# Kernel tuning notes

Measured on AMD Instinct MI355X. Metric: run time of the kernel, lower is better.

The kernel has to match this reference:

```python
import jax, jax.numpy as jnp
import numpy as np

B, X, Y, Z, C = 1, 16, 16, 16, 768
NUM_HEADS = 12


def setup_inputs() -> dict:
    key = jax.random.key(0)
    k0, k1, k2 = jax.random.split(key, 3)
    x = jax.random.normal(k0, (B, X, Y, Z, C), dtype=jnp.float32)
    # Linear weights stored as [in, out] (torch stores [out, in]; math is x @ W_in_out + b)
    w_qkv = jax.random.normal(k1, (C, 3 * C), dtype=jnp.float32) * 0.02
    b_qkv = jnp.zeros((3 * C,), dtype=jnp.float32)
    w_proj = jax.random.normal(k2, (C, C), dtype=jnp.float32) * 0.02
    b_proj = jnp.zeros((C,), dtype=jnp.float32)
    return {"x": x, "w_qkv": w_qkv, "b_qkv": b_qkv, "w_proj": w_proj, "b_proj": b_proj}


def reference(x, w_qkv, b_qkv, w_proj, b_proj):
    b, xx, yy, zz, c = x.shape
    h = NUM_HEADS
    hd = c // h
    scale = hd ** (-0.5)
    n = xx * yy * zz  # flatten 3D grid into tokens

    qkv = x.reshape(b, n, c) @ w_qkv + b_qkv          # [B, N, 3C]
    qkv = qkv.reshape(b, n, 3, h, hd).transpose(2, 0, 3, 1, 4)  # [3, B, H, N, hd]
    q, k, v = qkv[0], qkv[1], qkv[2]

    attn = jnp.einsum('bhnd,bhmd->bhnm', q * scale, k)  # [B, H, N, N]
    attn = jax.nn.softmax(attn, axis=-1)
    out = jnp.einsum('bhnm,bhmd->bhnd', attn, v)        # [B, H, N, hd]
    out = out.transpose(0, 2, 1, 3).reshape(b, n, c)
    out = out @ w_proj + b_proj
    return out.reshape(b, xx, yy, zz, c)
```

## Files before the change

### kernel.cpp

```cpp
#include <hip/hip_runtime.h>
#include <cstddef>

#define N_TOK 4096
#define C_DIM 768
#define H_NUM 12
#define C3    2304

typedef unsigned short u16;
using short8  = __attribute__((ext_vector_type(8))) short;
using floatx4 = __attribute__((ext_vector_type(4))) float;
using u16x4   = __attribute__((ext_vector_type(4))) u16;
using uint2v  = __attribute__((ext_vector_type(2))) unsigned;

#define K2SCALE 0.18033688011112043f

__device__ __forceinline__ u16 f2bf(float f) {
  union { float f; unsigned u; } v; v.f = f;
  unsigned r = v.u + 0x7FFFu + ((v.u >> 16) & 1u);
  return (u16)(r >> 16);
}

__device__ __forceinline__ unsigned permpack(float a, float b) {
  union { float f; unsigned u; } x, y; x.f = a; y.f = b;
  return __builtin_amdgcn_perm(y.u, x.u, 0x07060302u);
}

__device__ __forceinline__ float aexp2(float x) {
  float r;
  asm("v_exp_f32 %0, %1" : "=v"(r) : "v"(x));
  return r;
}

__device__ __forceinline__ float arcp(float x) {
  float r;
  asm("v_rcp_f32 %0, %1" : "=v"(r) : "v"(x));
  return r;
}

__device__ __forceinline__ void gload_lds16(const void* g, void* l) {
  __builtin_amdgcn_global_load_lds(
      (const __attribute__((address_space(1))) unsigned int*)g,
      (__attribute__((address_space(3))) unsigned int*)l, 16, 0, 0);
}

__global__ void k_pre(const float* __restrict__ x, u16* __restrict__ xb,
                      const float* __restrict__ wq, u16* __restrict__ wqT,
                      const float* __restrict__ wp, u16* __restrict__ wpT) {
  __shared__ float tile[32][33];
  const int b = blockIdx.x;
  if (b < 3072) {
    int i = b * 256 + threadIdx.x;
    float4 f = ((const float4*)x)[i];
    u16x4 o;
    o[0] = f2bf(f.x); o[1] = f2bf(f.y); o[2] = f2bf(f.z); o[3] = f2bf(f.w);
    ((u16x4*)xb)[i] = o;
    return;
  }
  const float* in; u16* out; int Cc, bx, by;
  if (b < 4800) { int t = b - 3072; in = wq; out = wqT; Cc = 2304; bx = t % 72; by = t / 72; }
  else          { int t = b - 4800; in = wp; out = wpT; Cc = 768;  bx = t % 24; by = t / 24; }
  const int R = 768;
  const int tx = threadIdx.x & 31;
  const int ty = threadIdx.x >> 5;
  const int c0 = bx * 32, r0 = by * 32;
#pragma unroll
  for (int i = 0; i < 32; i += 8)
    tile[ty + i][tx] = in[(size_t)(r0 + ty + i) * Cc + c0 + tx];
  __syncthreads();
#pragma unroll
  for (int i = 0; i < 32; i += 8)
    out[(size_t)(c0 + ty + i) * R + r0 + tx] = f2bf(tile[tx][ty + i]);
}

template <int MODE>
__global__ __launch_bounds__(256)
void k_gemm_bt(const u16* __restrict__ A, const u16* __restrict__ B,
               const float* __restrict__ bias, void* __restrict__ outp,
               u16* __restrict__ vT, int K) {
  __shared__ u16 As[128 * 32];
  __shared__ u16 Bs[128 * 32];
  const int tid  = threadIdx.x;
  const int wave = tid >> 6, lane = tid & 63, quad = lane >> 4, l16 = lane & 15;
  const int wrow = wave >> 1, wcol = wave & 1;
  const int bm = blockIdx.y, bn = blockIdx.x;
  const int r3 = l16 & 3;

  floatx4 acc[4][4];
#pragma unroll
  for (int i = 0; i < 4; ++i)
#pragma unroll
    for (int j = 0; j < 4; ++j)
#pragma unroll
      for (int r = 0; r < 4; ++r) acc[i][j][r] = 0.f;

  const int ar = tid >> 2;
  const int ac = ((tid & 3) ^ (ar & 3)) * 8;
  const u16* gA = A + (size_t)(bm * 128 + ar) * K + ac;
  const u16* gB = B + (size_t)(bn * 128 + ar) * K + ac;
  u16* lA = &As[0] + tid * 8;
  u16* lB = &Bs[0] + tid * 8;

  for (int k0 = 0; k0 < K; k0 += 32) {
    gload_lds16(gA + k0,                  lA);
    gload_lds16(gA + k0 + (size_t)64 * K, lA + 2048);
    gload_lds16(gB + k0,                  lB);
    gload_lds16(gB + k0 + (size_t)64 * K, lB + 2048);
    __syncthreads();
    short8 af[4], bf[4];
#pragma unroll
    for (int t = 0; t < 4; ++t) {
      af[t] = *(const short8*)&As[(wrow * 64 + t * 16 + l16) * 32 + ((quad ^ r3) * 8)];
      bf[t] = *(const short8*)&Bs[(wcol * 64 + t * 16 + l16) * 32 + ((quad ^ r3) * 8)];
    }
#pragma unroll
    for (int tm = 0; tm < 4; ++tm)
#pragma unroll
      for (int tn = 0; tn < 4; ++tn)
        acc[tm][tn] = __builtin_amdgcn_mfma_f32_16x16x32_bf16(af[tm], bf[tn], acc[tm][tn], 0, 0, 0);
    __syncthreads();
  }

  if (MODE == 0) {
    u16* qkv = (u16*)outp;
    const float qs = (bn < 6) ? K2SCALE : 1.0f;
#pragma unroll
    for (int tn = 0; tn < 4; ++tn) {
      const int col = bn * 128 + wcol * 64 + tn * 16 + l16;
      const float bc = bias[col];
      if (col < 1536) {
#pragma unroll
        for (int tm = 0; tm < 4; ++tm) {
          const int rowb = bm * 128 + wrow * 64 + tm * 16 + quad * 4;
#pragma unroll
          for (int r = 0; r < 4; ++r)
            qkv[(size_t)(rowb + r) * C3 + col] = f2bf((acc[tm][tn][r] + bc) * qs);
        }
      } else {
        const int hd_ = col - 1536;
#pragma unroll
        for (int tm = 0; tm < 4; ++tm) {
          const int rowb = bm * 128 + wrow * 64 + tm * 16 + quad * 4;
          u16x4 pk;
#pragma unroll
          for (int r = 0; r < 4; ++r) pk[r] = f2bf(acc[tm][tn][r] + bc);
          *(u16x4*)&vT[(size_t)hd_ * N_TOK + rowb] = pk;
        }
      }
    }
  } else {
    float* out = (float*)outp;
#pragma unroll
    for (int tn = 0; tn < 4; ++tn) {
      const int col = bn * 128 + wcol * 64 + tn * 16 + l16;
      const float bc = bias[col];
#pragma unroll
      for (int tm = 0; tm < 4; ++tm) {
        const int rowb = bm * 128 + wrow * 64 + tm * 16 + quad * 4;
#pragma unroll
        for (int r = 0; r < 4; ++r)
          out[(size_t)(rowb + r) * C_DIM + col] = acc[tm][tn][r] + bc;
      }
    }
  }
}

__global__ __launch_bounds__(256)
void k_flash(const u16* __restrict__ qkv, const u16* __restrict__ vT,
             float* __restrict__ Opart, float* __restrict__ lpart) {
  __shared__ u16 Ks[2][64 * 64];
  __shared__ u16 Vs[2][64 * 64];
  __shared__ u16 Ps[4][32 * 64];
  const int tid  = threadIdx.x;
  const int wave = tid >> 6, lane = tid & 63, quad = lane >> 4, l16 = lane & 15;
  const int qt = blockIdx.x, h = blockIdx.y, split = blockIdx.z;
  const int lr = tid >> 3;
  const int lc = ((tid & 7) ^ (lr & 7)) * 8;
  const int r7 = l16 & 7;
  const int kb = split * 2048;

  short8 bq[2][2];
#pragma unroll
  for (int qs = 0; qs < 2; ++qs)
#pragma unroll
    for (int ks = 0; ks < 2; ++ks)
      bq[qs][ks] = *(const short8*)&qkv[(size_t)(qt * 128 + wave * 32 + qs * 16 + l16) * C3
                                        + h * 64 + ks * 32 + quad * 8];

  const u16* gk = qkv + (size_t)lr * C3 + C_DIM + h * 64 + lc;
  const u16* gv = vT + (size_t)(h * 64 + lr) * N_TOK + lc;

  auto stage = [&](int b, int m0) {
#pragma unroll
    for (int p = 0; p < 2; ++p) {
      gload_lds16(gk + (size_t)(m0 + p * 32) * C3,    &Ks[b][p * 2048 + tid * 8]);
      gload_lds16(gv + (size_t)(p * 32) * N_TOK + m0, &Vs[b][p * 2048 + tid * 8]);
    }
  };

  floatx4 o0[4], o1[4], l0, l1, zv;
#pragma unroll
  for (int r = 0; r < 4; ++r) { zv[r] = 0.f; l0[r] = 0.f; l1[r] = 0.f; }
#pragma unroll
  for (int d = 0; d < 4; ++d)
#pragma unroll
    for (int r = 0; r < 4; ++r) { o0[d][r] = 0.f; o1[d][r] = 0.f; }

  short8 ones;
#pragma unroll
  for (int i = 0; i < 8; ++i) ones[i] = (short)0x3F80;

  u16* psw = &Ps[wave][0];

  auto compute = [&](int b) __attribute__((always_inline)) {
    const u16* kbp = &Ks[b][0];
    const u16* vb  = &Vs[b][0];
    floatx4 s0[4], s1[4];
#pragma unroll
    for (int tn = 0; tn < 4; ++tn) {
      short8 ak = *(const short8*)&kbp[(tn * 16 + l16) * 64 + (quad ^ r7) * 8];
      s0[tn] = __builtin_amdgcn_mfma_f32_16x16x32_bf16(ak, bq[0][0], zv, 0, 0, 0);
      s1[tn] = __builtin_amdgcn_mfma_f32_16x16x32_bf16(ak, bq[1][0], zv, 0, 0, 0);
    }
#pragma unroll
    for (int tn = 0; tn < 4; ++tn) {
      short8 ak = *(const short8*)&kbp[(tn * 16 + l16) * 64 + ((quad + 4) ^ r7) * 8];
      s0[tn] = __builtin_amdgcn_mfma_f32_16x16x32_bf16(ak, bq[0][1], s0[tn], 0, 0, 0);
      s1[tn] = __builtin_amdgcn_mfma_f32_16x16x32_bf16(ak, bq[1][1], s1[tn], 0, 0, 0);
    }
#pragma unroll
    for (int qs = 0; qs < 2; ++qs) {
      u16* pr = psw + qs * 1024;
#pragma unroll
      for (int tn = 0; tn < 4; ++tn) {
        floatx4 sv = qs ? s1[tn] : s0[tn];
        float p0 = aexp2(sv[0]);
        float p1 = aexp2(sv[1]);
        float p2 = aexp2(sv[2]);
        float p3 = aexp2(sv[3]);
        uint2v pk;
        pk[0] = permpack(p0, p1);
        pk[1] = permpack(p2, p3);
        *(uint2v*)&pr[l16 * 64 + ((2 * tn + (quad >> 1)) ^ r7) * 8 + (quad & 1) * 4] = pk;
      }
    }
#pragma unroll
    for (int ks = 0; ks < 2; ++ks) {
      short8 ap0 = *(const short8*)&psw[l16 * 64 + ((quad + 4 * ks) ^ r7) * 8];
      short8 ap1 = *(const short8*)&psw[(16 + l16) * 64 + ((quad + 4 * ks) ^ r7) * 8];
#pragma unroll
      for (int dt = 0; dt < 4; ++dt) {
        short8 bv = *(const short8*)&vb[(dt * 16 + l16) * 64 + ((quad + 4 * ks) ^ r7) * 8];
        o0[dt] = __builtin_amdgcn_mfma_f32_16x16x32_bf16(ap0, bv, o0[dt], 0, 0, 0);
        o1[dt] = __builtin_amdgcn_mfma_f32_16x16x32_bf16(ap1, bv, o1[dt], 0, 0, 0);
      }
      l0 = __builtin_amdgcn_mfma_f32_16x16x32_bf16(ap0, ones, l0, 0, 0, 0);
      l1 = __builtin_amdgcn_mfma_f32_16x16x32_bf16(ap1, ones, l1, 0, 0, 0);
    }
  };

  stage(0, kb);
  __syncthreads();
  int m0 = kb + 64;
  for (int it2 = 0; it2 < 15; ++it2) {
    stage(1, m0); m0 += 64;
    compute(0);
    __syncthreads();
    stage(0, m0); m0 += 64;
    compute(1);
    __syncthreads();
  }
  stage(1, m0);
  compute(0);
  __syncthreads();
  compute(1);

  const int rowg = qt * 128 + wave * 32 + quad * 4;
  float* Ob = Opart + ((size_t)(split * H_NUM + h) * N_TOK) * 64;
  float* lb = lpart + (size_t)(split * H_NUM + h) * N_TOK;
#pragma unroll
  for (int r = 0; r < 4; ++r) {
#pragma unroll
    for (int dt = 0; dt < 4; ++dt) {
      const int col = dt * 16 + l16;
      Ob[(size_t)(rowg + r) * 64 + col]      = o0[dt][r];
      Ob[(size_t)(rowg + 16 + r) * 64 + col] = o1[dt][r];
    }
    if (l16 == 0) {
      lb[rowg + r]      = l0[r];
      lb[rowg + 16 + r] = l1[r];
    }
  }
}

__global__ void k_combine(const float* __restrict__ Op, const float* __restrict__ lp,
                          u16* __restrict__ ao) {
  const int idx = blockIdx.x * 256 + threadIdx.x;
  const int col = idx & 63;
  const int row = idx >> 6;
  const float o = Op[(size_t)row * 64 + col] + Op[((size_t)row + 49152) * 64 + col];
  const float l = lp[row] + lp[row + 49152];
  const int h = row >> 12, q = row & 4095;
  ao[(size_t)q * C_DIM + h * 64 + col] = f2bf(o * arcp(l));
}

extern "C" void kernel_launch(void* const* d_in, const int* in_sizes, int n_in,
                              void* d_out, int out_size, void* d_ws, size_t ws_size,
                              hipStream_t stream) {
  const float* x      = (const float*)d_in[0];
  const float* w_qkv  = (const float*)d_in[1];
  const float* b_qkv  = (const float*)d_in[2];
  const float* w_proj = (const float*)d_in[3];
  const float* b_proj = (const float*)d_in[4];
  float* out = (float*)d_out;

  u16* xb     = (u16*)d_ws;
  u16* wqkvT  = xb     + (size_t)N_TOK * C_DIM;
  u16* wprojT = wqkvT  + (size_t)C3 * C_DIM;
  u16* qkv    = wprojT + (size_t)C_DIM * C_DIM;
  u16* vT     = qkv    + (size_t)N_TOK * C3;
  u16* ao     = vT     + (size_t)C_DIM * N_TOK;
  float* Opart = (float*)(ao + (size_t)N_TOK * C_DIM);
  float* lpart = Opart + (size_t)2 * H_NUM * N_TOK * 64;

  k_pre<<<5376, 256, 0, stream>>>(x, xb, w_qkv, wqkvT, w_proj, wprojT);
  k_gemm_bt<0><<<dim3(C3 / 128, N_TOK / 128), 256, 0, stream>>>(xb, wqkvT, b_qkv, qkv, vT, C_DIM);
  k_flash<<<dim3(N_TOK / 128, H_NUM, 2), 256, 0, stream>>>(qkv, vT, Opart, lpart);
  k_combine<<<H_NUM * N_TOK * 64 / 256, 256, 0, stream>>>(Opart, lpart, ao);
  k_gemm_bt<1><<<dim3(C_DIM / 128, N_TOK / 128), 256, 0, stream>>>(ao, wprojT, b_proj, out, nullptr, C_DIM);
}
```

Measured before the change: 216.7 us.

## Keep P in registers via permlane swaps, split KV four ways with atomic accumulation

The flash kernel no longer sends the softmax probabilities through LDS. It builds the PV MFMA operand in registers using permlane32/permlane16 swaps. The KV split goes from 2 to 4, and partial outputs and row sums are accumulated with float atomics into one zeroed buffer, which the preprocessing kernel now clears. It also adds s_setprio around the MFMA blocks and an occupancy hint in launch_bounds. This removes LDS traffic and barriers and raises the grid size, at the cost of atomic contention and an extra zeroing pass.

Result: faster. 203.7 us (-6.0%).

```diff
diff --git a/kernel.cpp b/kernel.cpp
--- a/kernel.cpp
+++ b/kernel.cpp
@@ -5,12 +5,13 @@
 #define C_DIM 768
 #define H_NUM 12
 #define C3    2304
+#define NSPLIT 4
 
 typedef unsigned short u16;
 using short8  = __attribute__((ext_vector_type(8))) short;
 using floatx4 = __attribute__((ext_vector_type(4))) float;
 using u16x4   = __attribute__((ext_vector_type(4))) u16;
-using uint2v  = __attribute__((ext_vector_type(2))) unsigned;
+using uint4v  = __attribute__((ext_vector_type(4))) unsigned;
 
 #define K2SCALE 0.18033688011112043f
 
@@ -37,6 +38,23 @@
   return r;
 }
 
+__device__ __forceinline__ void pl_swap32(unsigned &a, unsigned &b) {
+#if __has_builtin(__builtin_amdgcn_permlane32_swap)
+  auto r = __builtin_amdgcn_permlane32_swap(a, b, false, false);
+  a = r[0]; b = r[1];
+#else
+  asm("v_permlane32_swap_b32 %0, %1" : "+v"(a), "+v"(b));
+#endif
+}
+__device__ __forceinline__ void pl_swap16(unsigned &a, unsigned &b) {
+#if __has_builtin(__builtin_amdgcn_permlane16_swap)
+  auto r = __builtin_amdgcn_permlane16_swap(a, b, false, false);
+  a = r[0]; b = r[1];
+#else
+  asm("v_permlane16_swap_b32 %0, %1" : "+v"(a), "+v"(b));
+#endif
+}
+
 __device__ __forceinline__ void gload_lds16(const void* g, void* l) {
   __builtin_amdgcn_global_load_lds(
       (const __attribute__((address_space(1))) unsigned int*)g,
@@ -45,9 +63,16 @@
 
 __global__ void k_pre(const float* __restrict__ x, u16* __restrict__ xb,
                       const float* __restrict__ wq, u16* __restrict__ wqT,
-                      const float* __restrict__ wp, u16* __restrict__ wpT) {
+                      const float* __restrict__ wp, u16* __restrict__ wpT,
+                      float* __restrict__ Oz) {
   __shared__ float tile[32][33];
   const int b = blockIdx.x;
+  if (b >= 5376) {
+    size_t i = (size_t)(b - 5376) * 256 + threadIdx.x;
+    float4 z; z.x = 0.f; z.y = 0.f; z.z = 0.f; z.w = 0.f;
+    ((float4*)Oz)[i] = z;
+    return;
+  }
   if (b < 3072) {
     int i = b * 256 + threadIdx.x;
     float4 f = ((const float4*)x)[i];
@@ -164,19 +189,18 @@
   }
 }
 
-__global__ __launch_bounds__(256)
+__global__ __launch_bounds__(256, 4)
 void k_flash(const u16* __restrict__ qkv, const u16* __restrict__ vT,
              float* __restrict__ Opart, float* __restrict__ lpart) {
   __shared__ u16 Ks[2][64 * 64];
   __shared__ u16 Vs[2][64 * 64];
-  __shared__ u16 Ps[4][32 * 64];
   const int tid  = threadIdx.x;
   const int wave = tid >> 6, lane = tid & 63, quad = lane >> 4, l16 = lane & 15;
   const int qt = blockIdx.x, h = blockIdx.y, split = blockIdx.z;
   const int lr = tid >> 3;
   const int lc = ((tid & 7) ^ (lr & 7)) * 8;
   const int r7 = l16 & 7;
-  const int kb = split * 2048;
+  const int kb = split * 1024;
 
   short8 bq[2][2];
 #pragma unroll
@@ -208,13 +232,12 @@
   short8 ones;
 #pragma unroll
   for (int i = 0; i < 8; ++i) ones[i] = (short)0x3F80;
-
-  u16* psw = &Ps[wave][0];
 
   auto compute = [&](int b) __attribute__((always_inline)) {
     const u16* kbp = &Ks[b][0];
     const u16* vb  = &Vs[b][0];
     floatx4 s0[4], s1[4];
+    __builtin_amdgcn_s_setprio(1);
 #pragma unroll
     for (int tn = 0; tn < 4; ++tn) {
       short8 ak = *(const short8*)&kbp[(tn * 16 + l16) * 64 + (quad ^ r7) * 8];
@@ -227,26 +250,36 @@
       s0[tn] = __builtin_amdgcn_mfma_f32_16x16x32_bf16(ak, bq[0][1], s0[tn], 0, 0, 0);
       s1[tn] = __builtin_amdgcn_mfma_f32_16x16x32_bf16(ak, bq[1][1], s1[tn], 0, 0, 0);
     }
-#pragma unroll
-    for (int qs = 0; qs < 2; ++qs) {
-      u16* pr = psw + qs * 1024;
-#pragma unroll
-      for (int tn = 0; tn < 4; ++tn) {
-        floatx4 sv = qs ? s1[tn] : s0[tn];
-        float p0 = aexp2(sv[0]);
-        float p1 = aexp2(sv[1]);
-        float p2 = aexp2(sv[2]);
-        float p3 = aexp2(sv[3]);
-        uint2v pk;
-        pk[0] = permpack(p0, p1);
-        pk[1] = permpack(p2, p3);
-        *(uint2v*)&pr[l16 * 64 + ((2 * tn + (quad >> 1)) ^ r7) * 8 + (quad & 1) * 4] = pk;
+    __builtin_amdgcn_s_setprio(0);
+
+    unsigned pk0[4][2], pk1[4][2];
+#pragma unroll
+    for (int tn = 0; tn < 4; ++tn) {
+      pk0[tn][0] = permpack(aexp2(s0[tn][0]), aexp2(s0[tn][1]));
+      pk0[tn][1] = permpack(aexp2(s0[tn][2]), aexp2(s0[tn][3]));
+      pk1[tn][0] = permpack(aexp2(s1[tn][0]), aexp2(s1[tn][1]));
+      pk1[tn][1] = permpack(aexp2(s1[tn][2]), aexp2(s1[tn][3]));
+    }
+#pragma unroll
+    for (int t1 = 0; t1 < 2; ++t1)
+#pragma unroll
+      for (int w = 0; w < 2; ++w) {
+        pl_swap32(pk0[2 * t1][w], pk0[2 * t1 + 1][w]);
+        pl_swap16(pk0[2 * t1][w], pk0[2 * t1 + 1][w]);
+        pl_swap32(pk1[2 * t1][w], pk1[2 * t1 + 1][w]);
+        pl_swap16(pk1[2 * t1][w], pk1[2 * t1 + 1][w]);
       }
-    }
+
 #pragma unroll
     for (int ks = 0; ks < 2; ++ks) {
-      short8 ap0 = *(const short8*)&psw[l16 * 64 + ((quad + 4 * ks) ^ r7) * 8];
-      short8 ap1 = *(const short8*)&psw[(16 + l16) * 64 + ((quad + 4 * ks) ^ r7) * 8];
+      uint4v t0v, t1v;
+      t0v[0] = pk0[2 * ks][0]; t0v[1] = pk0[2 * ks][1];
+      t0v[2] = pk0[2 * ks + 1][0]; t0v[3] = pk0[2 * ks + 1][1];
+      t1v[0] = pk1[2 * ks][0]; t1v[1] = pk1[2 * ks][1];
+      t1v[2] = pk1[2 * ks + 1][0]; t1v[3] = pk1[2 * ks + 1][1];
+      const short8 ap0 = __builtin_bit_cast(short8, t0v);
+      const short8 ap1 = __builtin_bit_cast(short8, t1v);
+      __builtin_amdgcn_s_setprio(1);
 #pragma unroll
       for (int dt = 0; dt < 4; ++dt) {
         short8 bv = *(const short8*)&vb[(dt * 16 + l16) * 64 + ((quad + 4 * ks) ^ r7) * 8];
@@ -255,13 +288,14 @@
       }
       l0 = __builtin_amdgcn_mfma_f32_16x16x32_bf16(ap0, ones, l0, 0, 0, 0);
       l1 = __builtin_amdgcn_mfma_f32_16x16x32_bf16(ap1, ones, l1, 0, 0, 0);
+      __builtin_amdgcn_s_setprio(0);
     }
   };
 
   stage(0, kb);
   __syncthreads();
   int m0 = kb + 64;
-  for (int it2 = 0; it2 < 15; ++it2) {
+  for (int it2 = 0; it2 < 7; ++it2) {
     stage(1, m0); m0 += 64;
     compute(0);
     __syncthreads();
@@ -275,19 +309,19 @@
   compute(1);
 
   const int rowg = qt * 128 + wave * 32 + quad * 4;
-  float* Ob = Opart + ((size_t)(split * H_NUM + h) * N_TOK) * 64;
-  float* lb = lpart + (size_t)(split * H_NUM + h) * N_TOK;
+  float* Ob = Opart + (size_t)h * N_TOK * 64;
+  float* lb = lpart + (size_t)h * N_TOK;
 #pragma unroll
   for (int r = 0; r < 4; ++r) {
 #pragma unroll
     for (int dt = 0; dt < 4; ++dt) {
       const int col = dt * 16 + l16;
-      Ob[(size_t)(rowg + r) * 64 + col]      = o0[dt][r];
-      Ob[(size_t)(rowg + 16 + r) * 64 + col] = o1[dt][r];
+      atomicAdd(&Ob[(size_t)(rowg + r) * 64 + col],      o0[dt][r]);
+      atomicAdd(&Ob[(size_t)(rowg + 16 + r) * 64 + col], o1[dt][r]);
     }
     if (l16 == 0) {
-      lb[rowg + r]      = l0[r];
-      lb[rowg + 16 + r] = l1[r];
+      atomicAdd(&lb[rowg + r],      l0[r]);
+      atomicAdd(&lb[rowg + 16 + r], l1[r]);
     }
   }
 }
@@ -297,8 +331,8 @@
   const int idx = blockIdx.x * 256 + threadIdx.x;
   const int col = idx & 63;
   const int row = idx >> 6;
-  const float o = Op[(size_t)row * 64 + col] + Op[((size_t)row + 49152) * 64 + col];
-  const float l = lp[row] + lp[row + 49152];
+  const float o = Op[(size_t)row * 64 + col];
+  const float l = lp[row];
   const int h = row >> 12, q = row & 4095;
   ao[(size_t)q * C_DIM + h * 64 + col] = f2bf(o * arcp(l));
 }
@@ -320,11 +354,11 @@
   u16* vT     = qkv    + (size_t)N_TOK * C3;
   u16* ao     = vT     + (size_t)C_DIM * N_TOK;
   float* Opart = (float*)(ao + (size_t)N_TOK * C_DIM);
-  float* lpart = Opart + (size_t)2 * H_NUM * N_TOK * 64;
-
-  k_pre<<<5376, 256, 0, stream>>>(x, xb, w_qkv, wqkvT, w_proj, wprojT);
+  float* lpart = Opart + (size_t)H_NUM * N_TOK * 64;
+
+  k_pre<<<8496, 256, 0, stream>>>(x, xb, w_qkv, wqkvT, w_proj, wprojT, Opart);
   k_gemm_bt<0><<<dim3(C3 / 128, N_TOK / 128), 256, 0, stream>>>(xb, wqkvT, b_qkv, qkv, vT, C_DIM);
-  k_flash<<<dim3(N_TOK / 128, H_NUM, 2), 256, 0, stream>>>(qkv, vT, Opart, lpart);
+  k_flash<<<dim3(N_TOK / 128, H_NUM, NSPLIT), 256, 0, stream>>>(qkv, vT, Opart, lpart);
   k_combine<<<H_NUM * N_TOK * 64 / 256, 256, 0, stream>>>(Opart, lpart, ao);
   k_gemm_bt<1><<<dim3(C_DIM / 128, N_TOK / 128), 256, 0, stream>>>(ao, wprojT, b_proj, out, nullptr, C_DIM);
 }
```
